# Kernel tuning notes

Measured on AMD Instinct MI355X. Metric: run time of the kernel, lower is better.

## Reference

```python
import jax, jax.numpy as jnp
import numpy as np

N, C, R, K = 128, 1001, 51, 10          # rois, classes, relations, topk proposals
ROUNDS = 3                                # cfg.TEST.REL_INFER_ROUND
W_BGREL = 1.0                             # cfg.REL_INFER.NONE_BGREL_WEIGHT
W_BIN = 1.0                               # cfg.TEST.REL_INFER_BINARY_WEIGHT
MIX = 10000.0                             # scatter blending weight


def setup_inputs() -> dict:
    key = jax.random.key(0)
    k1, k2, k3 = jax.random.split(key, 3)
    # roi class scores (probabilities, positive so log is finite)
    roi_scores = jax.random.uniform(k1, (N, C), dtype=jnp.float32, minval=0.01, maxval=1.0)
    # pairwise relation log-scores (exp'd inside forward since REL_INFER.TRAIN=False)
    rel_scores = jax.random.normal(k2, (N * N, R), dtype=jnp.float32)
    # dense relationship co-occurrence matrix; channel 0 (background rel) filled with 1
    relationship_mat = jax.random.uniform(k3, (C, C, R), dtype=jnp.float32)
    relationship_mat = relationship_mat.at[:, :, 0].set(1.0)
    return {"roi_scores": roi_scores, "rel_scores": rel_scores,
            "relationship_mat": relationship_mat}


def reference(roi_scores, rel_scores, relationship_mat):
    n = roi_scores.shape[0]
    # rel_scores -> probabilities (not-train path)
    rel = jnp.exp(rel_scores).reshape(n, n, -1)          # [N,N,R]
    topk_scores, topk_labels = jax.lax.top_k(roi_scores, K)  # [N,K]
    flat = topk_labels.reshape(-1)                        # [N*K]
    # gather pairwise potentials for every (label_i, label_j) pair
    bt = relationship_mat[flat[:, None], flat[None, :]]   # [NK,NK,R]
    bt = bt.reshape(n, K, n, K, -1) * rel[:, None, :, None, :]
    # combine background relation (channel 0) with non-bg relations (MODE != 3 -> sum)
    bt = bt[..., 0] + W_BGREL * bt[..., 1:].sum(-1)       # [N,K,N,K]
    bt = (bt + bt.transpose(2, 3, 0, 1)) * 0.5            # symmetrize over roi pairs
    bt = jnp.log(bt)
    # zero the self-pair (i == j) block: torch.diagonal(bt, dim1=0, dim2=2).fill_(0)
    bt = jnp.where(jnp.eye(n, dtype=bool)[:, None, :, None], 0.0, bt)
    unary = jnp.log(topk_scores)                          # [N,K]
    Q = jnp.full((n, K), 1.0 / K, dtype=roi_scores.dtype) # softmax of ones
    for _ in range(ROUNDS):
        msg = jnp.einsum('akbl,bl->ak', bt, Q)            # mean-field message
        Q = jax.nn.softmax(W_BIN * msg + unary, axis=1)
    new_roi = jnp.zeros_like(roi_scores).at[jnp.arange(n)[:, None], topk_labels].set(Q)
    return (roi_scores + MIX * new_roi) / (1.0 + MIX)
```

## Files before the change

kernel.cpp:

```cpp
#include <hip/hip_runtime.h>
#include <hip/hip_bf16.h>

#define NN 128
#define CC 1001
#define RR 51
#define KK 10
#define NK (NN*KK)
#define BT_ELEMS (NN*KK*NN*KK)
#define W_BIN_C 1.0f
#define MIX_C 10000.0f

typedef float f4_t __attribute__((ext_vector_type(4)));
typedef f4_t f4u __attribute__((aligned(4)));

__global__ __launch_bounds__(64) void topk_kernel(const float* __restrict__ roi,
                                                  int* __restrict__ labels,
                                                  float* __restrict__ unary) {
    int a = blockIdx.x, lane = threadIdx.x;
    const float* rowp = roi + a * CC;
    float v[16];
    #pragma unroll
    for (int j = 0; j < 16; ++j) {
        int c = lane + 64 * j;
        v[j] = (c < CC) ? rowp[c] : -1e30f;
    }
    for (int k = 0; k < KK; ++k) {
        float bv = v[0]; int bj = 0;
        #pragma unroll
        for (int j = 1; j < 16; ++j) if (v[j] > bv) { bv = v[j]; bj = j; }
        int bc = lane + 64 * bj;
        #pragma unroll
        for (int m = 32; m > 0; m >>= 1) {
            float v2 = __shfl_xor(bv, m, 64);
            int   c2 = __shfl_xor(bc, m, 64);
            if (v2 > bv || (v2 == bv && c2 < bc)) { bv = v2; bc = c2; }
        }
        if (lane == (bc & 63)) {
            int j = bc >> 6;
            #pragma unroll
            for (int jj = 0; jj < 16; ++jj) if (jj == j) v[jj] = -1e30f;
        }
        if (lane == 0) {
            labels[a * KK + k] = bc;
            unary[a * KK + k]  = logf(bv);
        }
    }
}

__global__ __launch_bounds__(256) void pair_kernel(const float* __restrict__ rel_scores,
                                                   const float* __restrict__ relmat,
                                                   const int* __restrict__ labels,
                                                   float* __restrict__ bt) {
    int a = blockIdx.y, b = blockIdx.x;
    if (a > b) return;
    int t = threadIdx.x;
    if (a == b) {
        if (t < 100) {
            int k = t / 10, l = t % 10;
            bt[((a * KK + k) * NN + a) * KK + l] = 0.0f;
        }
        return;
    }

    __shared__ int   La[KK], Lb[KK];
    __shared__ int   baseAB[100], baseBA[100], oAB[100], oBA[100];
    __shared__ float eAB[RR], eBA[RR];

    if (t < KK)            La[t]      = labels[a * KK + t];
    else if (t < 2 * KK)   Lb[t - KK] = labels[b * KK + (t - KK)];
    if (t >= 64  && t < 64 + RR)  eAB[t - 64]  = expf(rel_scores[(a * NN + b) * RR + (t - 64)]);
    if (t >= 128 && t < 128 + RR) eBA[t - 128] = expf(rel_scores[(b * NN + a) * RR + (t - 128)]);
    __syncthreads();
    if (t < 100) {
        int k = t / 10, l = t % 10;
        baseAB[t] = (La[k] * CC + Lb[l]) * RR;
        baseBA[t] = (Lb[l] * CC + La[k]) * RR;
        oAB[t]    = ((a * KK + k) * NN + b) * KK + l;
        oBA[t]    = ((b * KK + l) * NN + a) * KK + k;
    }
    __syncthreads();

    int gid = t >> 3;
    int sub = t & 7;
    bool act0 = sub < 7, act1 = sub < 6;
    int r0 = (sub < 6) ? sub * 8 : 47;
    int r1 = sub * 8 + 4;

    f4_t zero; zero.x = zero.y = zero.z = zero.w = 0.f;
    f4_t c0A = zero, c1A = zero, c0B = zero, c1B = zero;
    if (sub < 6) {
        c0A.x = eAB[r0];   c0A.y = eAB[r0+1]; c0A.z = eAB[r0+2]; c0A.w = eAB[r0+3];
        c1A.x = eAB[r1];   c1A.y = eAB[r1+1]; c1A.z = eAB[r1+2]; c1A.w = eAB[r1+3];
        c0B.x = eBA[r0];   c0B.y = eBA[r0+1]; c0B.z = eBA[r0+2]; c0B.w = eBA[r0+3];
        c1B.x = eBA[r1];   c1B.y = eBA[r1+1]; c1B.z = eBA[r1+2]; c1B.w = eBA[r1+3];
    } else if (sub == 6) {
        c0A.x = 0.f; c0A.y = eAB[48]; c0A.z = eAB[49]; c0A.w = eAB[50];
        c0B.x = 0.f; c0B.y = eBA[48]; c0B.z = eBA[49]; c0B.w = eBA[50];
    }

    f4_t A0[4], A1[4], B0[4], B1[4];
    #pragma unroll
    for (int u = 0; u < 4; ++u) {
        int kl = gid + 32 * u;
        bool h = (kl < 100);
        int kls = h ? kl : 0;
        int bA = baseAB[kls], bB = baseBA[kls];
        A0[u] = (h && act0) ? *(const f4u*)(relmat + bA + r0) : zero;
        A1[u] = (h && act1) ? *(const f4u*)(relmat + bA + r1) : zero;
        B0[u] = (h && act0) ? *(const f4u*)(relmat + bB + r0) : zero;
        B1[u] = (h && act1) ? *(const f4u*)(relmat + bB + r1) : zero;
    }
    float s[4];
    #pragma unroll
    for (int u = 0; u < 4; ++u) {
        s[u] = A0[u].x*c0A.x + A0[u].y*c0A.y + A0[u].z*c0A.z + A0[u].w*c0A.w
             + A1[u].x*c1A.x + A1[u].y*c1A.y + A1[u].z*c1A.z + A1[u].w*c1A.w
             + B0[u].x*c0B.x + B0[u].y*c0B.y + B0[u].z*c0B.z + B0[u].w*c0B.w
             + B1[u].x*c1B.x + B1[u].y*c1B.y + B1[u].z*c1B.z + B1[u].w*c1B.w;
    }
    #pragma unroll
    for (int m = 4; m > 0; m >>= 1) {
        #pragma unroll
        for (int u = 0; u < 4; ++u) s[u] += __shfl_xor(s[u], m, 64);
    }
    if (sub == 0) {
        #pragma unroll
        for (int u = 0; u < 4; ++u) {
            int kl = gid + 32 * u;
            if (kl < 100) {
                float vv = logf(0.5f * s[u]);
                bt[oAB[kl]] = vv;
                bt[oBA[kl]] = vv;
            }
        }
    }
}

__global__ __launch_bounds__(640) void round_kernel(const float* __restrict__ bt,
                                                    const float* __restrict__ unary,
                                                    const float* __restrict__ Qin,
                                                    float* __restrict__ Qout,
                                                    int uniform) {
    int a = blockIdx.x, t = threadIdx.x;
    int wave = t >> 6, lane = t & 63;
    __shared__ float sQ[NK];
    __shared__ float smsg[KK];
    if (!uniform && t < NK / 4) ((f4_t*)sQ)[t] = ((const f4_t*)Qin)[t];
    __syncthreads();
    const f4_t* row = (const f4_t*)(bt + (a * KK + wave) * NK);
    float acc = 0.f;
    if (uniform) {
        #pragma unroll
        for (int j = 0; j < 5; ++j) {
            f4_t r = row[lane + 64 * j];
            acc += r.x + r.y + r.z + r.w;
        }
        acc *= (1.0f / (float)KK);
    } else {
        const f4_t* q4 = (const f4_t*)sQ;
        #pragma unroll
        for (int j = 0; j < 5; ++j) {
            f4_t r = row[lane + 64 * j];
            f4_t q = q4[lane + 64 * j];
            acc += r.x * q.x + r.y * q.y + r.z * q.z + r.w * q.w;
        }
    }
    #pragma unroll
    for (int m = 32; m > 0; m >>= 1) acc += __shfl_xor(acc, m, 64);
    if (lane == 0) smsg[wave] = acc;
    __syncthreads();
    if (t == 0) {
        float e[KK], m = -1e30f;
        #pragma unroll
        for (int k = 0; k < KK; ++k) {
            float v = W_BIN_C * smsg[k] + unary[a * KK + k];
            e[k] = v;
            if (v > m) m = v;
        }
        float s = 0.f;
        #pragma unroll
        for (int k = 0; k < KK; ++k) { e[k] = expf(e[k] - m); s += e[k]; }
        #pragma unroll
        for (int k = 0; k < KK; ++k) Qout[a * KK + k] = e[k] / s;
    }
}

__global__ __launch_bounds__(640) void round_out_kernel(const float* __restrict__ bt,
                                                        const float* __restrict__ unary,
                                                        const float* __restrict__ Qin,
                                                        const float* __restrict__ roi,
                                                        const int* __restrict__ labels,
                                                        float* __restrict__ out) {
    int a = blockIdx.x, t = threadIdx.x;
    int wave = t >> 6, lane = t & 63;
    __shared__ float sQ[NK];
    __shared__ float smsg[KK];
    __shared__ float sq[KK];
    __shared__ int   sL[KK];
    if (t < NK / 4) ((f4_t*)sQ)[t] = ((const f4_t*)Qin)[t];
    if (t >= 320 && t < 320 + KK) sL[t - 320] = labels[a * KK + (t - 320)];
    __syncthreads();
    const f4_t* row = (const f4_t*)(bt + (a * KK + wave) * NK);
    const f4_t* q4  = (const f4_t*)sQ;
    float acc = 0.f;
    #pragma unroll
    for (int j = 0; j < 5; ++j) {
        f4_t r = row[lane + 64 * j];
        f4_t q = q4[lane + 64 * j];
        acc += r.x * q.x + r.y * q.y + r.z * q.z + r.w * q.w;
    }
    #pragma unroll
    for (int m = 32; m > 0; m >>= 1) acc += __shfl_xor(acc, m, 64);
    if (lane == 0) smsg[wave] = acc;
    __syncthreads();
    if (t == 0) {
        float e[KK], m = -1e30f;
        #pragma unroll
        for (int k = 0; k < KK; ++k) {
            float v = W_BIN_C * smsg[k] + unary[a * KK + k];
            e[k] = v;
            if (v > m) m = v;
        }
        float s = 0.f;
        #pragma unroll
        for (int k = 0; k < KK; ++k) { e[k] = expf(e[k] - m); s += e[k]; }
        #pragma unroll
        for (int k = 0; k < KK; ++k) sq[k] = e[k] / s;
    }
    __syncthreads();
    for (int c = t; c < CC; c += 640) {
        float q = 0.f;
        #pragma unroll
        for (int k = 0; k < KK; ++k) if (sL[k] == c) q = sq[k];
        out[a * CC + c] = (roi[a * CC + c] + MIX_C * q) / (1.0f + MIX_C);
    }
}

extern "C" void kernel_launch(void* const* d_in, const int* in_sizes, int n_in,
                              void* d_out, int out_size, void* d_ws, size_t ws_size,
                              hipStream_t stream) {
    const float* roi    = (const float*)d_in[0];
    const float* rel    = (const float*)d_in[1];
    const float* relmat = (const float*)d_in[2];
    float* out = (float*)d_out;

    char* ws = (char*)d_ws;
    float* bt     = (float*)ws;
    int*   labels = (int*)(ws + (size_t)BT_ELEMS * 4);
    float* unary  = (float*)(ws + (size_t)BT_ELEMS * 4 + 5120);
    float* QA     = unary + NK;
    float* QB     = QA + NK;

    topk_kernel<<<NN, 64, 0, stream>>>(roi, labels, unary);
    pair_kernel<<<dim3(NN, NN), 256, 0, stream>>>(rel, relmat, labels, bt);
    round_kernel<<<NN, 640, 0, stream>>>(bt, unary, QA, QA, 1);
    round_kernel<<<NN, 640, 0, stream>>>(bt, unary, QA, QB, 0);
    round_out_kernel<<<NN, 640, 0, stream>>>(bt, unary, QB, roi, labels, out);
}
```

Measured before the change: 94.95 us.

## Invert pairwise gather into a class-pair scatter over relationship matrix rows

Replaces the per-ROI-pair gather of relationship_mat rows with a pass over all class-pair rows. Each row used by some pair of top-k labels is read once and its relation-weighted sum is scattered to every (a,k,b,l) occurrence, using per-class occurrence lists built with atomics in the top-k kernel. exp of rel_scores is precomputed once, and the symmetrize, log and diagonal zeroing move into a separate elementwise pass. This is meant to cut redundant random reads of the large relationship matrix. In exchange it launches a grid covering every class pair, most of which exit early, and it caps occurrences per class at 32, which would give wrong results if a class appeared more often.

```diff
diff --git a/kernel.cpp b/kernel.cpp
--- a/kernel.cpp
+++ b/kernel.cpp
@@ -7,16 +7,36 @@
 #define KK 10
 #define NK (NN*KK)
 #define BT_ELEMS (NN*KK*NN*KK)
+#define NROWS (CC*CC)
+#define MAXO 32
 #define W_BIN_C 1.0f
 #define MIX_C 10000.0f
 
 typedef float f4_t __attribute__((ext_vector_type(4)));
 typedef f4_t f4u __attribute__((aligned(4)));
 
-__global__ __launch_bounds__(64) void topk_kernel(const float* __restrict__ roi,
-                                                  int* __restrict__ labels,
-                                                  float* __restrict__ unary) {
-    int a = blockIdx.x, lane = threadIdx.x;
+__global__ __launch_bounds__(256) void prep_kernel(const float* __restrict__ roi,
+                                                   const float* __restrict__ rel,
+                                                   float* __restrict__ exp_rel,
+                                                   int* __restrict__ labels,
+                                                   float* __restrict__ unary,
+                                                   int* __restrict__ count,
+                                                   int* __restrict__ list) {
+    int blk = blockIdx.x;
+    if (blk < 104) {
+        const f4_t* in4 = (const f4_t*)rel;
+        f4_t* out4 = (f4_t*)exp_rel;
+        for (int i = blk * 256 + threadIdx.x; i < (NN * NN * RR) / 4; i += 104 * 256) {
+            f4_t v = in4[i];
+            f4_t e;
+            e.x = expf(v.x); e.y = expf(v.y); e.z = expf(v.z); e.w = expf(v.w);
+            out4[i] = e;
+        }
+        return;
+    }
+    int a = blk - 104;
+    int lane = threadIdx.x;
+    if (lane >= 64) return;
     const float* rowp = roi + a * CC;
     float v[16];
     #pragma unroll
@@ -43,97 +63,70 @@
         if (lane == 0) {
             labels[a * KK + k] = bc;
             unary[a * KK + k]  = logf(bv);
-        }
-    }
-}
-
-__global__ __launch_bounds__(256) void pair_kernel(const float* __restrict__ rel_scores,
-                                                   const float* __restrict__ relmat,
-                                                   const int* __restrict__ labels,
-                                                   float* __restrict__ bt) {
-    int a = blockIdx.y, b = blockIdx.x;
-    if (a > b) return;
+            int slot = atomicAdd(&count[bc], 1);
+            if (slot < MAXO) list[bc * MAXO + slot] = (a << 4) | k;
+        }
+    }
+}
+
+__global__ __launch_bounds__(256) void scatter_kernel(const float* __restrict__ relmat,
+                                                      const float* __restrict__ exp_rel,
+                                                      const int* __restrict__ count,
+                                                      const int* __restrict__ list,
+                                                      float* __restrict__ raw) {
     int t = threadIdx.x;
-    if (a == b) {
-        if (t < 100) {
-            int k = t / 10, l = t % 10;
-            bt[((a * KK + k) * NN + a) * KK + l] = 0.0f;
-        }
-        return;
-    }
-
-    __shared__ int   La[KK], Lb[KK];
-    __shared__ int   baseAB[100], baseBA[100], oAB[100], oBA[100];
-    __shared__ float eAB[RR], eBA[RR];
-
-    if (t < KK)            La[t]      = labels[a * KK + t];
-    else if (t < 2 * KK)   Lb[t - KK] = labels[b * KK + (t - KK)];
-    if (t >= 64  && t < 64 + RR)  eAB[t - 64]  = expf(rel_scores[(a * NN + b) * RR + (t - 64)]);
-    if (t >= 128 && t < 128 + RR) eBA[t - 128] = expf(rel_scores[(b * NN + a) * RR + (t - 128)]);
-    __syncthreads();
-    if (t < 100) {
-        int k = t / 10, l = t % 10;
-        baseAB[t] = (La[k] * CC + Lb[l]) * RR;
-        baseBA[t] = (Lb[l] * CC + La[k]) * RR;
-        oAB[t]    = ((a * KK + k) * NN + b) * KK + l;
-        oBA[t]    = ((b * KK + l) * NN + a) * KK + k;
-    }
-    __syncthreads();
-
-    int gid = t >> 3;
-    int sub = t & 7;
+    int g = t >> 3, sub = t & 7;
+    int R = blockIdx.x * 32 + g;
+    if (R >= NROWS) return;
+    int x = R / CC, y = R % CC;
+    int nx = count[x]; if (nx == 0) return;
+    int ny = count[y]; if (ny == 0) return;
+    if (nx > MAXO) nx = MAXO;
+    if (ny > MAXO) ny = MAXO;
+
     bool act0 = sub < 7, act1 = sub < 6;
     int r0 = (sub < 6) ? sub * 8 : 47;
     int r1 = sub * 8 + 4;
-
     f4_t zero; zero.x = zero.y = zero.z = zero.w = 0.f;
-    f4_t c0A = zero, c1A = zero, c0B = zero, c1B = zero;
-    if (sub < 6) {
-        c0A.x = eAB[r0];   c0A.y = eAB[r0+1]; c0A.z = eAB[r0+2]; c0A.w = eAB[r0+3];
-        c1A.x = eAB[r1];   c1A.y = eAB[r1+1]; c1A.z = eAB[r1+2]; c1A.w = eAB[r1+3];
-        c0B.x = eBA[r0];   c0B.y = eBA[r0+1]; c0B.z = eBA[r0+2]; c0B.w = eBA[r0+3];
-        c1B.x = eBA[r1];   c1B.y = eBA[r1+1]; c1B.z = eBA[r1+2]; c1B.w = eBA[r1+3];
-    } else if (sub == 6) {
-        c0A.x = 0.f; c0A.y = eAB[48]; c0A.z = eAB[49]; c0A.w = eAB[50];
-        c0B.x = 0.f; c0B.y = eBA[48]; c0B.z = eBA[49]; c0B.w = eBA[50];
-    }
-
-    f4_t A0[4], A1[4], B0[4], B1[4];
-    #pragma unroll
-    for (int u = 0; u < 4; ++u) {
-        int kl = gid + 32 * u;
-        bool h = (kl < 100);
-        int kls = h ? kl : 0;
-        int bA = baseAB[kls], bB = baseBA[kls];
-        A0[u] = (h && act0) ? *(const f4u*)(relmat + bA + r0) : zero;
-        A1[u] = (h && act1) ? *(const f4u*)(relmat + bA + r1) : zero;
-        B0[u] = (h && act0) ? *(const f4u*)(relmat + bB + r0) : zero;
-        B1[u] = (h && act1) ? *(const f4u*)(relmat + bB + r1) : zero;
-    }
-    float s[4];
-    #pragma unroll
-    for (int u = 0; u < 4; ++u) {
-        s[u] = A0[u].x*c0A.x + A0[u].y*c0A.y + A0[u].z*c0A.z + A0[u].w*c0A.w
-             + A1[u].x*c1A.x + A1[u].y*c1A.y + A1[u].z*c1A.z + A1[u].w*c1A.w
-             + B0[u].x*c0B.x + B0[u].y*c0B.y + B0[u].z*c0B.z + B0[u].w*c0B.w
-             + B1[u].x*c1B.x + B1[u].y*c1B.y + B1[u].z*c1B.z + B1[u].w*c1B.w;
-    }
-    #pragma unroll
-    for (int m = 4; m > 0; m >>= 1) {
-        #pragma unroll
-        for (int u = 0; u < 4; ++u) s[u] += __shfl_xor(s[u], m, 64);
-    }
-    if (sub == 0) {
-        #pragma unroll
-        for (int u = 0; u < 4; ++u) {
-            int kl = gid + 32 * u;
-            if (kl < 100) {
-                float vv = logf(0.5f * s[u]);
-                bt[oAB[kl]] = vv;
-                bt[oBA[kl]] = vv;
-            }
-        }
-    }
+    const float* rowp = relmat + R * RR;
+    f4_t c0 = act0 ? *(const f4u*)(rowp + r0) : zero;
+    f4_t c1 = act1 ? *(const f4u*)(rowp + r1) : zero;
+    if (sub == 6) c0.x = 0.f;
+
+    for (int i = 0; i < nx; ++i) {
+        int ea = list[x * MAXO + i];
+        int a = ea >> 4, k = ea & 15;
+        int obase = (a * KK + k) * NK;
+        const float* epbase = exp_rel + a * (NN * RR);
+        for (int j = 0; j < ny; ++j) {
+            int eb = list[y * MAXO + j];
+            int b = eb >> 4, l = eb & 15;
+            const float* ep = epbase + b * RR;
+            f4_t e0 = act0 ? *(const f4u*)(ep + r0) : zero;
+            f4_t e1 = act1 ? *(const f4u*)(ep + r1) : zero;
+            float s = c0.x*e0.x + c0.y*e0.y + c0.z*e0.z + c0.w*e0.w
+                    + c1.x*e1.x + c1.y*e1.y + c1.z*e1.z + c1.w*e1.w;
+            s += __shfl_xor(s, 4, 64);
+            s += __shfl_xor(s, 2, 64);
+            s += __shfl_xor(s, 1, 64);
+            if (sub == 0) raw[obase + b * KK + l] = s;
+        }
+    }
+}
+
+__global__ __launch_bounds__(256) void symlog_kernel(float* __restrict__ bt) {
+    int i = blockIdx.x * 256 + threadIdx.x;
+    int l = i % KK;
+    int b = (i / KK) % NN;
+    int k = (i / (KK * NN)) % KK;
+    int a = i / (KK * NN * KK);
+    if (a > b) return;
+    if (a == b) { bt[i] = 0.0f; return; }
+    int j = ((b * KK + l) * NN + a) * KK + k;
+    float xx = bt[i], yy = bt[j];
+    float v = logf(0.5f * (xx + yy));
+    bt[i] = v;
+    bt[j] = v;
 }
 
 __global__ __launch_bounds__(640) void round_kernel(const float* __restrict__ bt,
@@ -245,14 +238,20 @@
     float* out = (float*)d_out;
 
     char* ws = (char*)d_ws;
-    float* bt     = (float*)ws;
-    int*   labels = (int*)(ws + (size_t)BT_ELEMS * 4);
-    float* unary  = (float*)(ws + (size_t)BT_ELEMS * 4 + 5120);
-    float* QA     = unary + NK;
-    float* QB     = QA + NK;
-
-    topk_kernel<<<NN, 64, 0, stream>>>(roi, labels, unary);
-    pair_kernel<<<dim3(NN, NN), 256, 0, stream>>>(rel, relmat, labels, bt);
+    size_t off = 0;
+    float* bt      = (float*)(ws + off); off += (size_t)BT_ELEMS * 4;
+    float* exp_rel = (float*)(ws + off); off += (size_t)NN * NN * RR * 4;
+    int*   labels  = (int*)(ws + off);   off += NK * 4;
+    float* unary   = (float*)(ws + off); off += NK * 4;
+    float* QA      = (float*)(ws + off); off += NK * 4;
+    float* QB      = (float*)(ws + off); off += NK * 4;
+    int*   count   = (int*)(ws + off);   off += ((CC * 4 + 15) / 16) * 16;
+    int*   list    = (int*)(ws + off);   off += (size_t)CC * MAXO * 4;
+
+    hipMemsetAsync(count, 0, CC * sizeof(int), stream);
+    prep_kernel<<<104 + NN, 256, 0, stream>>>(roi, rel, exp_rel, labels, unary, count, list);
+    scatter_kernel<<<(NROWS + 31) / 32, 256, 0, stream>>>(relmat, exp_rel, count, list, bt);
+    symlog_kernel<<<BT_ELEMS / 256, 256, 0, stream>>>(bt);
     round_kernel<<<NN, 640, 0, stream>>>(bt, unary, QA, QA, 1);
     round_kernel<<<NN, 640, 0, stream>>>(bt, unary, QA, QB, 0);
     round_out_kernel<<<NN, 640, 0, stream>>>(bt, unary, QB, roi, labels, out);
```

Result: slower. 150.9 us (+58.9%).
